# Kernel optimization log

Measured on AMD Instinct MI355X. Metric: run time of the kernel, lower is better.

Reference implementation:

```python
import jax, jax.numpy as jnp
import numpy as np

B = 2
D = 256
NH = 8
DH = D // NH
LV = 4
NP_ = 4
NL = 6
DFF = 1024
SHAPES = [(112, 112), (56, 56), (28, 28), (14, 14)]
S = sum(h * w for h, w in SHAPES)


def setup_inputs() -> dict:
    key = jax.random.key(0)
    ks = iter(jax.random.split(key, 64))
    d = {}
    for i, (h, w) in enumerate(SHAPES):
        d[f"src{i}"] = jax.random.normal(next(ks), (B, D, h, w), jnp.float32)
        d[f"pos{i}"] = jax.random.normal(next(ks), (B, D, h, w), jnp.float32)

    def W(*shape, scale=0.02):
        return jax.random.normal(next(ks), shape, jnp.float32) * scale

    d["level_embed"] = W(LV, D, scale=1.0)
    d["off_w"] = W(NL, D, NH * LV * NP_ * 2)
    d["off_b"] = W(NL, NH * LV * NP_ * 2, scale=0.5)
    d["aw_w"] = W(NL, D, NH * LV * NP_)
    d["aw_b"] = jnp.zeros((NL, NH * LV * NP_), jnp.float32)
    d["val_w"] = W(NL, D, D)
    d["val_b"] = jnp.zeros((NL, D), jnp.float32)
    d["out_w"] = W(NL, D, D)
    d["out_b"] = jnp.zeros((NL, D), jnp.float32)
    d["ln1_s"] = jnp.ones((NL, D), jnp.float32)
    d["ln1_b"] = jnp.zeros((NL, D), jnp.float32)
    d["ff1_w"] = W(NL, D, DFF)
    d["ff1_b"] = jnp.zeros((NL, DFF), jnp.float32)
    d["ff2_w"] = W(NL, DFF, D)
    d["ff2_b"] = jnp.zeros((NL, D), jnp.float32)
    d["ln2_s"] = jnp.ones((NL, D), jnp.float32)
    d["ln2_b"] = jnp.zeros((NL, D), jnp.float32)
    return d


def _ln(x, s, b):
    m = jnp.mean(x, -1, keepdims=True)
    v = jnp.mean((x - m) ** 2, -1, keepdims=True)
    return (x - m) / jnp.sqrt(v + 1e-5) * s + b


def _bilinear(v, loc, Hl, Wl):
    # v: [N, DH, Hl, Wl]; loc: [N, Q, P, 2] in [0,1] (grid_sample align_corners=False, zero padding)
    N, Dh = v.shape[0], v.shape[1]
    Q, P = loc.shape[1], loc.shape[2]
    x = loc[..., 0] * Wl - 0.5
    y = loc[..., 1] * Hl - 0.5
    x0f = jnp.floor(x)
    y0f = jnp.floor(y)
    lx = x - x0f
    ly = y - y0f
    x0 = x0f.astype(jnp.int32)
    y0 = y0f.astype(jnp.int32)
    vf = v.reshape(N, Dh, Hl * Wl)

    def g(xi, yi):
        valid = (xi >= 0) & (xi < Wl) & (yi >= 0) & (yi < Hl)
        idx = (jnp.clip(yi, 0, Hl - 1) * Wl + jnp.clip(xi, 0, Wl - 1)).reshape(N, Q * P)
        out = jnp.take_along_axis(vf, idx[:, None, :], axis=2).reshape(N, Dh, Q, P)
        return out * valid[:, None].astype(v.dtype)

    w00 = ((1 - lx) * (1 - ly))[:, None]
    w10 = (lx * (1 - ly))[:, None]
    w01 = ((1 - lx) * ly)[:, None]
    w11 = (lx * ly)[:, None]
    return g(x0, y0) * w00 + g(x0 + 1, y0) * w10 + g(x0, y0 + 1) * w01 + g(x0 + 1, y0 + 1) * w11


def _ms_deform_attn(value, loc, attn):
    # value [B,S,NH,DH], loc [B,S,NH,LV,P,2], attn [B,S,NH,LV,P]
    out = jnp.zeros((B * NH, DH, S), value.dtype)
    s0 = 0
    for l, (Hl, Wl) in enumerate(SHAPES):
        vl = value[:, s0:s0 + Hl * Wl].reshape(B, Hl, Wl, NH, DH)
        vl = vl.transpose(0, 3, 4, 1, 2).reshape(B * NH, DH, Hl, Wl)
        ll = loc[:, :, :, l].transpose(0, 2, 1, 3, 4).reshape(B * NH, S, NP_, 2)
        al = attn[:, :, :, l].transpose(0, 2, 1, 3).reshape(B * NH, S, NP_)[:, None]
        out = out + (_bilinear(vl, ll, Hl, Wl) * al).sum(-1)
        s0 += Hl * Wl
    return out.reshape(B, NH * DH, S).transpose(0, 2, 1)


def _forward(srcs, poss, level_embed, off_w, off_b, aw_w, aw_b, val_w, val_b,
             out_w, out_b, ln1_s, ln1_b, ff1_w, ff1_b, ff2_w, ff2_b, ln2_s, ln2_b):
    src = jnp.concatenate([s.reshape(B, D, -1).transpose(0, 2, 1) for s in srcs], 1)
    pos = jnp.concatenate(
        [p.reshape(B, D, -1).transpose(0, 2, 1) + level_embed[i][None, None] for i, p in enumerate(poss)], 1)
    # reference points: padding masks are all-False => valid_ratios == 1
    refs = []
    for (Hl, Wl) in SHAPES:
        gy, gx = jnp.meshgrid((jnp.arange(Hl) + 0.5) / Hl, (jnp.arange(Wl) + 0.5) / Wl, indexing="ij")
        refs.append(jnp.stack([gx.ravel(), gy.ravel()], -1))
    ref = jnp.concatenate(refs, 0)  # [S, 2]
    normalizer = jnp.array([[w, h] for (h, w) in SHAPES], jnp.float32)  # [LV, 2] = (W, H)
    x = src
    for i in range(NL):
        q = x + pos
        off = (q @ off_w[i] + off_b[i]).reshape(B, S, NH, LV, NP_, 2)
        aw = jax.nn.softmax((q @ aw_w[i] + aw_b[i]).reshape(B, S, NH, LV * NP_), -1)
        aw = aw.reshape(B, S, NH, LV, NP_)
        val = (x @ val_w[i] + val_b[i]).reshape(B, S, NH, DH)
        loc = ref[None, :, None, None, None, :] + off / normalizer[None, None, None, :, None, :]
        attn_out = _ms_deform_attn(val, loc, aw) @ out_w[i] + out_b[i]
        x = _ln(x + attn_out, ln1_s[i], ln1_b[i])
        ff = jax.nn.relu(x @ ff1_w[i] + ff1_b[i]) @ ff2_w[i] + ff2_b[i]
        x = _ln(x + ff, ln2_s[i], ln2_b[i])
    return x


def reference(src0, src1, src2, src3, pos0, pos1, pos2, pos3, level_embed,
              off_w, off_b, aw_w, aw_b, val_w, val_b, out_w, out_b,
              ln1_s, ln1_b, ff1_w, ff1_b, ff2_w, ff2_b, ln2_s, ln2_b):
    memory = _forward([src0, src1, src2, src3], [pos0, pos1, pos2, pos3], level_embed,
                      off_w, off_b, aw_w, aw_b, val_w, val_b, out_w, out_b,
                      ln1_s, ln1_b, ff1_w, ff1_b, ff2_w, ff2_b, ln2_s, ln2_b)
    spatial_shapes = jnp.array(SHAPES, jnp.int32)
    level_start_index = jnp.concatenate(
        [jnp.zeros((1,), jnp.int32), jnp.cumsum(spatial_shapes.prod(1))[:-1].astype(jnp.int32)])
    return memory, spatial_shapes, level_start_index
```

## Files before the change

### kernel.cpp

```cpp
#include <hip/hip_runtime.h>


constexpr int kB  = 2;
constexpr int kD  = 256;
constexpr int kNH = 8;
constexpr int kLV = 4;
constexpr int kNP = 4;
constexpr int kNL = 6;
constexpr int kDFF = 1024;
constexpr int kS  = 16660;
constexpr int kM  = kB * kS;
constexpr int kMp = 33408;
constexpr int kMT64 = kMp / 64;
constexpr int kMT32 = kMp / 32;

typedef short bf16x8 __attribute__((ext_vector_type(8)));
typedef float f32x4  __attribute__((ext_vector_type(4)));

__device__ __forceinline__ unsigned short f2bf(float x) {
  union { float f; unsigned int u; } v; v.f = x;
  unsigned int r = v.u + 0x7FFFu + ((v.u >> 16) & 1u);
  return (unsigned short)(r >> 16);
}
__device__ __forceinline__ float bf2f(unsigned short u) {
  union { unsigned int u; float f; } v; v.u = ((unsigned int)u) << 16;
  return v.f;
}
__device__ __forceinline__ float bflo(unsigned int u) {
  union { unsigned int u; float f; } v; v.u = u << 16;
  return v.f;
}
__device__ __forceinline__ float bfhi(unsigned int u) {
  union { unsigned int u; float f; } v; v.u = u & 0xFFFF0000u;
  return v.f;
}

#define GLOAD_LDS16(gp, lp)                                                    \
  __builtin_amdgcn_global_load_lds(                                            \
      (const __attribute__((address_space(1))) void*)(gp),                     \
      (__attribute__((address_space(3))) void*)(lp), 16, 0, 0)

__global__ __launch_bounds__(256) void build_xpos_k(
    const float* __restrict__ src, const float* __restrict__ pos,
    const float* __restrict__ lemb, float* __restrict__ xout,
    float* __restrict__ posout, unsigned short* __restrict__ xbf,
    unsigned short* __restrict__ qbf, int HW, int s0, int lvl)
{
  __shared__ float ts[32][33];
  __shared__ float tp[32][33];
  const int b  = blockIdx.z;
  const int p0 = blockIdx.x * 32, d0 = blockIdx.y * 32;
  const int tx = threadIdx.x, ty = threadIdx.y;
  for (int dd = ty; dd < 32; dd += 8) {
    int p = p0 + tx;
    if (p < HW) {
      size_t idx = ((size_t)b * kD + (d0 + dd)) * (size_t)HW + p;
      ts[dd][tx] = src[idx];
      tp[dd][tx] = pos[idx];
    }
  }
  __syncthreads();
  for (int pp = ty; pp < 32; pp += 8) {
    int p = p0 + pp, d = d0 + tx;
    if (p < HW) {
      size_t o = ((size_t)b * kS + (s0 + p)) * (size_t)kD + d;
      float x = ts[tx][pp];
      float pv = tp[tx][pp] + lemb[lvl * kD + d];
      xout[o] = x;
      posout[o] = pv;
      xbf[o] = f2bf(x);
      qbf[o] = f2bf(x + pv);
    }
  }
}

__global__ __launch_bounds__(256) void wconv_k(
    const float* __restrict__ W, unsigned short* __restrict__ Wt,
    int K, int N, int rowoff, int rowstotal)
{
  __shared__ float t[32][33];
  const int l = blockIdx.z;
  const int n0 = blockIdx.x * 32, k0 = blockIdx.y * 32;
  const int tx = threadIdx.x & 31, ty = threadIdx.x >> 5;
  const float* Wl = W + (size_t)l * K * N;
  unsigned short* Wtl = Wt + (size_t)l * rowstotal * K;
  for (int kk = ty; kk < 32; kk += 8)
    t[kk][tx] = Wl[(size_t)(k0 + kk) * N + n0 + tx];
  __syncthreads();
  for (int nn = ty; nn < 32; nn += 8)
    Wtl[(size_t)(rowoff + n0 + nn) * K + k0 + tx] = f2bf(t[tx][nn]);
}

__global__ __launch_bounds__(256) void biaspack_k(
    const float* __restrict__ ob, const float* __restrict__ ab,
    float* __restrict__ qb)
{
  int i = blockIdx.x * 256 + threadIdx.x;
  if (i >= kNL * 384) return;
  int l = i / 384, c = i - l * 384;
  qb[i] = (c < 256) ? ob[l * 256 + c] : ab[l * 128 + (c - 256)];
}

__global__ __launch_bounds__(256) void refxy_k(float* __restrict__ ref)
{
  int s = blockIdx.x * 256 + threadIdx.x;
  if (s >= kS) return;
  int ls, side;
  if (s < 12544)      { ls = s;         side = 112; }
  else if (s < 15680) { ls = s - 12544; side = 56;  }
  else if (s < 16464) { ls = s - 15680; side = 28;  }
  else                { ls = s - 16464; side = 14;  }
  const float inv = 1.0f / (float)side;
  ref[s * 2 + 0] = ((ls % side) + 0.5f) * inv;
  ref[s * 2 + 1] = ((ls / side) + 0.5f) * inv;
}

template<int RELU, int OUTBF>
__global__ __launch_bounds__(256) void hgemm64_k(
    const unsigned short* __restrict__ A, const unsigned short* __restrict__ Bt,
    const float* __restrict__ bias, void* __restrict__ Cout, int N, int K)
{
  __shared__ unsigned short As[2][64 * 32];
  __shared__ unsigned short Bs[2][128 * 32];
  const int tid = threadIdx.x;
  const int bm = blockIdx.y * 64;
  const int bn = blockIdx.x * 128;
  const int lane = tid & 63;
  const int wave = tid >> 6;
  const int wr = (wave >> 1) * 32, wc = (wave & 1) * 64;
  const int l15 = lane & 15, l4 = lane >> 4;

  f32x4 acc[2][4] = {};

  const unsigned short* A0 = A + (size_t)(bm + (tid >> 2)) * K + ((tid & 3) << 3);
  const int cb1 = 256 + tid;
  const unsigned short* B0 = Bt + (size_t)(bn + (tid >> 2)) * K + ((tid & 3) << 3);
  const unsigned short* B1 = Bt + (size_t)(bn + (cb1 >> 2)) * K + ((cb1 & 3) << 3);

#define STAGE64(buf, k0)                                                       \
  do {                                                                         \
    GLOAD_LDS16(A0 + (k0), (char*)As[buf] + tid * 16);                         \
    GLOAD_LDS16(B0 + (k0), (char*)Bs[buf] + tid * 16);                         \
    GLOAD_LDS16(B1 + (k0), (char*)Bs[buf] + cb1 * 16);                         \
  } while (0)

  STAGE64(0, 0);
  __syncthreads();
  int cur = 0;
  for (int k0 = 0; k0 < K; k0 += 32) {
    if (k0 + 32 < K) STAGE64(cur ^ 1, k0 + 32);
    bf16x8 af[2], bfr[4];
#pragma unroll
    for (int m = 0; m < 2; ++m)
      af[m] = *(const bf16x8*)&As[cur][(wr + m * 16 + l15) * 32 + l4 * 8];
#pragma unroll
    for (int n = 0; n < 4; ++n)
      bfr[n] = *(const bf16x8*)&Bs[cur][(wc + n * 16 + l15) * 32 + l4 * 8];
#pragma unroll
    for (int m = 0; m < 2; ++m)
#pragma unroll
      for (int n = 0; n < 4; ++n)
        acc[m][n] = __builtin_amdgcn_mfma_f32_16x16x32_bf16(
            af[m], bfr[n], acc[m][n], 0, 0, 0);
    __syncthreads();
    cur ^= 1;
  }
#undef STAGE64

#pragma unroll
  for (int n = 0; n < 4; ++n) {
    const int col = bn + wc + n * 16 + l15;
    const float bv = bias[col];
#pragma unroll
    for (int m = 0; m < 2; ++m) {
#pragma unroll
      for (int j = 0; j < 4; ++j) {
        const int row = bm + wr + m * 16 + l4 * 4 + j;
        float v = acc[m][n][j] + bv;
        if (RELU) v = fmaxf(v, 0.f);
        if (OUTBF)
          ((unsigned short*)Cout)[(size_t)row * N + col] = f2bf(v);
        else
          ((float*)Cout)[(size_t)row * N + col] = v;
      }
    }
  }
}

__global__ __launch_bounds__(256) void qvgemm_k(
    const unsigned short* __restrict__ Aq, const unsigned short* __restrict__ Ax,
    const unsigned short* __restrict__ Bq, const unsigned short* __restrict__ Bv,
    const float* __restrict__ biasq, const float* __restrict__ biasv,
    float* __restrict__ Cq, unsigned short* __restrict__ Cv)
{
  constexpr int K = 256;
  __shared__ unsigned short As[2][64 * 32];
  __shared__ unsigned short Bs[2][128 * 32];
  const int tid = threadIdx.x;
  const int bx = blockIdx.x;
  const bool isv = bx >= 3;
  const int bn = (isv ? bx - 3 : bx) * 128;
  const int bm = blockIdx.y * 64;
  const unsigned short* A  = isv ? Ax : Aq;
  const unsigned short* Bt = isv ? Bv : Bq;
  const float* bias = isv ? biasv : biasq;
  const int lane = tid & 63;
  const int wave = tid >> 6;
  const int wr = (wave >> 1) * 32, wc = (wave & 1) * 64;
  const int l15 = lane & 15, l4 = lane >> 4;

  f32x4 acc[2][4] = {};

  const unsigned short* A0 = A + (size_t)(bm + (tid >> 2)) * K + ((tid & 3) << 3);
  const int cb1 = 256 + tid;
  const unsigned short* B0 = Bt + (size_t)(bn + (tid >> 2)) * K + ((tid & 3) << 3);
  const unsigned short* B1 = Bt + (size_t)(bn + (cb1 >> 2)) * K + ((cb1 & 3) << 3);

#define STAGEQV(buf, k0)                                                       \
  do {                                                                         \
    GLOAD_LDS16(A0 + (k0), (char*)As[buf] + tid * 16);                         \
    GLOAD_LDS16(B0 + (k0), (char*)Bs[buf] + tid * 16);                         \
    GLOAD_LDS16(B1 + (k0), (char*)Bs[buf] + cb1 * 16);                         \
  } while (0)

  STAGEQV(0, 0);
  __syncthreads();
  int cur = 0;
#pragma unroll
  for (int k0 = 0; k0 < K; k0 += 32) {
    if (k0 + 32 < K) STAGEQV(cur ^ 1, k0 + 32);
    bf16x8 af[2], bfr[4];
#pragma unroll
    for (int m = 0; m < 2; ++m)
      af[m] = *(const bf16x8*)&As[cur][(wr + m * 16 + l15) * 32 + l4 * 8];
#pragma unroll
    for (int n = 0; n < 4; ++n)
      bfr[n] = *(const bf16x8*)&Bs[cur][(wc + n * 16 + l15) * 32 + l4 * 8];
#pragma unroll
    for (int m = 0; m < 2; ++m)
#pragma unroll
      for (int n = 0; n < 4; ++n)
        acc[m][n] = __builtin_amdgcn_mfma_f32_16x16x32_bf16(
            af[m], bfr[n], acc[m][n], 0, 0, 0);
    __syncthreads();
    cur ^= 1;
  }
#undef STAGEQV

#pragma unroll
  for (int n = 0; n < 4; ++n) {
    const int col = bn + wc + n * 16 + l15;
    const float bv = bias[col];
#pragma unroll
    for (int m = 0; m < 2; ++m) {
#pragma unroll
      for (int j = 0; j < 4; ++j) {
        const int row = bm + wr + m * 16 + l4 * 4 + j;
        float v = acc[m][n][j] + bv;
        if (isv)
          Cv[(size_t)row * 256 + col] = f2bf(v);
        else
          Cq[(size_t)row * 384 + col] = v;
      }
    }
  }
}

template<int WQ, int OUTDST>
__global__ __launch_bounds__(256) void hgemmln_k(
    const unsigned short* __restrict__ A, const unsigned short* __restrict__ Bt,
    const float* __restrict__ bias, const float* __restrict__ Rsd,
    const float* __restrict__ g, const float* __restrict__ beta,
    const float* __restrict__ posb, float* __restrict__ yout,
    unsigned short* __restrict__ xbf, unsigned short* __restrict__ qbf, int K)
{
  __shared__ unsigned short As[2][32 * 32];
  __shared__ unsigned short Bs[2][256 * 32];
  __shared__ float ssum[32][5];
  __shared__ float ssq[32][5];
  const int tid = threadIdx.x;
  const int bm = blockIdx.x * 32;
  const int lane = tid & 63;
  const int wave = tid >> 6;
  const int wc = wave * 64;
  const int l15 = lane & 15, l4 = lane >> 4;

  f32x4 acc[2][4] = {};

  const unsigned short* Aq = A + (size_t)(bm + (tid >> 2)) * K + ((tid & 3) << 3);
  const unsigned short* Bq0 = Bt + (size_t)(0 * 64 + (tid >> 2)) * K + ((tid & 3) << 3);
  const unsigned short* Bq1 = Bt + (size_t)(1 * 64 + (tid >> 2)) * K + ((tid & 3) << 3);
  const unsigned short* Bq2 = Bt + (size_t)(2 * 64 + (tid >> 2)) * K + ((tid & 3) << 3);
  const unsigned short* Bq3 = Bt + (size_t)(3 * 64 + (tid >> 2)) * K + ((tid & 3) << 3);

#define STAGE_LN(buf, k0)                                                      \
  do {                                                                         \
    if (tid < 128) GLOAD_LDS16(Aq + (k0), (char*)As[buf] + tid * 16);          \
    GLOAD_LDS16(Bq0 + (k0), (char*)Bs[buf] + (0 * 256 + tid) * 16);            \
    GLOAD_LDS16(Bq1 + (k0), (char*)Bs[buf] + (1 * 256 + tid) * 16);            \
    GLOAD_LDS16(Bq2 + (k0), (char*)Bs[buf] + (2 * 256 + tid) * 16);            \
    GLOAD_LDS16(Bq3 + (k0), (char*)Bs[buf] + (3 * 256 + tid) * 16);            \
  } while (0)

  STAGE_LN(0, 0);
  __syncthreads();
  int cur = 0;
  for (int k0 = 0; k0 < K; k0 += 32) {
    if (k0 + 32 < K) STAGE_LN(cur ^ 1, k0 + 32);
    bf16x8 af[2], bfr[4];
#pragma unroll
    for (int m = 0; m < 2; ++m)
      af[m] = *(const bf16x8*)&As[cur][(m * 16 + l15) * 32 + l4 * 8];
#pragma unroll
    for (int n = 0; n < 4; ++n)
      bfr[n] = *(const bf16x8*)&Bs[cur][(wc + n * 16 + l15) * 32 + l4 * 8];
#pragma unroll
    for (int m = 0; m < 2; ++m)
#pragma unroll
      for (int n = 0; n < 4; ++n)
        acc[m][n] = __builtin_amdgcn_mfma_f32_16x16x32_bf16(
            af[m], bfr[n], acc[m][n], 0, 0, 0);
    __syncthreads();
    cur ^= 1;
  }
#undef STAGE_LN

  float bv[4], gv[4], btv[4];
#pragma unroll
  for (int n = 0; n < 4; ++n) {
    const int col = wc + n * 16 + l15;
    bv[n] = bias[col];
    gv[n] = g[col];
    btv[n] = beta[col];
  }
#pragma unroll
  for (int m = 0; m < 2; ++m) {
#pragma unroll
    for (int j = 0; j < 4; ++j) {
      const int row = bm + m * 16 + l4 * 4 + j;
#pragma unroll
      for (int n = 0; n < 4; ++n)
        acc[m][n][j] += bv[n] + Rsd[(size_t)row * kD + wc + n * 16 + l15];
    }
  }
#pragma unroll
  for (int m = 0; m < 2; ++m) {
#pragma unroll
    for (int j = 0; j < 4; ++j) {
      float s = acc[m][0][j] + acc[m][1][j] + acc[m][2][j] + acc[m][3][j];
      float q = acc[m][0][j] * acc[m][0][j] + acc[m][1][j] * acc[m][1][j] +
                acc[m][2][j] * acc[m][2][j] + acc[m][3][j] * acc[m][3][j];
#pragma unroll
      for (int d2 = 1; d2 < 16; d2 <<= 1) {
        s += __shfl_xor(s, d2, 64);
        q += __shfl_xor(q, d2, 64);
      }
      if (l15 == 0) {
        const int r = m * 16 + l4 * 4 + j;
        ssum[r][wave] = s;
        ssq[r][wave] = q;
      }
    }
  }
  __syncthreads();
#pragma unroll
  for (int m = 0; m < 2; ++m) {
#pragma unroll
    for (int j = 0; j < 4; ++j) {
      const int r = m * 16 + l4 * 4 + j;
      const int row = bm + r;
      const float mean = (ssum[r][0] + ssum[r][1] + ssum[r][2] + ssum[r][3]) *
                         (1.0f / kD);
      const float var = (ssq[r][0] + ssq[r][1] + ssq[r][2] + ssq[r][3]) *
                        (1.0f / kD) - mean * mean;
      const float rstd = rsqrtf(var + 1e-5f);
      if (row < kM) {
#pragma unroll
        for (int n = 0; n < 4; ++n) {
          const int col = wc + n * 16 + l15;
          const float y = (acc[m][n][j] - mean) * rstd * gv[n] + btv[n];
          const size_t o = (size_t)row * kD + col;
          if (OUTDST) {
            yout[o] = y;
          } else {
            yout[o] = y;
            xbf[o] = f2bf(y);
            if (WQ) qbf[o] = f2bf(y + posb[o]);
          }
        }
      }
    }
  }
}

__global__ __launch_bounds__(256) void msdeform_k(
    const unsigned short* __restrict__ val, const float* __restrict__ qout,
    const float* __restrict__ ref, unsigned short* __restrict__ outbf)
{
  __shared__ int   sIdx[4][8][128];
  __shared__ float sW[4][8][128];
  const int bs0 = blockIdx.x * 8;
  const int tid = threadIdx.x;

#pragma unroll
  for (int it = 0; it < 4; ++it) {
    const int item = tid + it * 256;
    const int q = item >> 7;
    const int t = item & 127;
    const int bs = bs0 + q;
    const int b = bs / kS, s = bs - b * kS;
    const int l = (t & 15) >> 2;

    const float logit = qout[(size_t)bs * 384 + 256 + t];
    float mx = logit;
#pragma unroll
    for (int d2 = 1; d2 < 16; d2 <<= 1) mx = fmaxf(mx, __shfl_xor(mx, d2, 64));
    float e = __expf(logit - mx);
    float sm = e;
#pragma unroll
    for (int d2 = 1; d2 < 16; d2 <<= 1) sm += __shfl_xor(sm, d2, 64);
    const float a = e / sm;

    const float rfx = ref[s * 2 + 0];
    const float rfy = ref[s * 2 + 1];
    const int side  = 112 >> l;
    const int start = (l >= 1 ? 12544 : 0) + (l >= 2 ? 3136 : 0) + (l >= 3 ? 784 : 0);
    const float ox = qout[(size_t)bs * 384 + t * 2 + 0];
    const float oy = qout[(size_t)bs * 384 + t * 2 + 1];
    const float xx = fmaf(rfx, (float)side, ox) - 0.5f;
    const float yy = fmaf(rfy, (float)side, oy) - 0.5f;
    const float xf = floorf(xx), yf = floorf(yy);
    const float lx = xx - xf, ly = yy - yf;
    const int x0 = (int)xf, y0 = (int)yf;
    const float w00 = (1.f - lx) * (1.f - ly) * a, w10 = lx * (1.f - ly) * a;
    const float w01 = (1.f - lx) * ly * a,         w11 = lx * ly * a;
    const bool xv0 = (unsigned)x0 < (unsigned)side, xv1 = (unsigned)(x0 + 1) < (unsigned)side;
    const bool yv0 = (unsigned)y0 < (unsigned)side, yv1 = (unsigned)(y0 + 1) < (unsigned)side;
    const int cx0 = min(max(x0, 0), side - 1), cx1 = min(max(x0 + 1, 0), side - 1);
    const int cy0 = min(max(y0, 0), side - 1), cy1 = min(max(y0 + 1, 0), side - 1);
    const int rowbase = b * kS + start;
    const int t2 = (t & 15) * 8 + (t >> 4);
    sIdx[0][q][t2] = (rowbase + cy0 * side + cx0) << 9;
    sIdx[1][q][t2] = (rowbase + cy0 * side + cx1) << 9;
    sIdx[2][q][t2] = (rowbase + cy1 * side + cx0) << 9;
    sIdx[3][q][t2] = (rowbase + cy1 * side + cx1) << 9;
    sW[0][q][t2] = (xv0 && yv0) ? w00 : 0.f;
    sW[1][q][t2] = (xv1 && yv0) ? w10 : 0.f;
    sW[2][q][t2] = (xv0 && yv1) ? w01 : 0.f;
    sW[3][q][t2] = (xv1 && yv1) ? w11 : 0.f;
  }
  __syncthreads();

  const int q  = tid >> 5;
  const int h  = (tid >> 2) & 7;
  const int l4 = tid & 3;
  const char* vbase = (const char*)val + h * 64 + l4 * 16;

  float a0 = 0.f, a1 = 0.f, a2 = 0.f, a3 = 0.f;
  float a4 = 0.f, a5 = 0.f, a6 = 0.f, a7 = 0.f;
#pragma unroll
  for (int sp = 0; sp < 16; ++sp) {
    const int t2 = sp * 8 + h;
#pragma unroll
    for (int c = 0; c < 4; ++c) {
      const int off = sIdx[c][q][t2];
      const float w = sW[c][q][t2];
      const uint4 v = *(const uint4*)(vbase + off);
      a0 = fmaf(w, bflo(v.x), a0); a1 = fmaf(w, bfhi(v.x), a1);
      a2 = fmaf(w, bflo(v.y), a2); a3 = fmaf(w, bfhi(v.y), a3);
      a4 = fmaf(w, bflo(v.z), a4); a5 = fmaf(w, bfhi(v.z), a5);
      a6 = fmaf(w, bflo(v.w), a6); a7 = fmaf(w, bfhi(v.w), a7);
    }
  }
  bf16x8 o;
  o[0] = (short)f2bf(a0); o[1] = (short)f2bf(a1);
  o[2] = (short)f2bf(a2); o[3] = (short)f2bf(a3);
  o[4] = (short)f2bf(a4); o[5] = (short)f2bf(a5);
  o[6] = (short)f2bf(a6); o[7] = (short)f2bf(a7);
  *(bf16x8*)(outbf + (size_t)(bs0 + q) * 256 + h * 32 + l4 * 8) = o;
}

__global__ void tail_k(float* __restrict__ out)
{
  if (threadIdx.x == 0) {
    const size_t n = (size_t)kM * kD;
    out[n + 0] = 112.f; out[n + 1] = 112.f;
    out[n + 2] = 56.f;  out[n + 3] = 56.f;
    out[n + 4] = 28.f;  out[n + 5] = 28.f;
    out[n + 6] = 14.f;  out[n + 7] = 14.f;
    out[n + 8] = 0.f;   out[n + 9] = 12544.f;
    out[n + 10] = 15680.f; out[n + 11] = 16464.f;
  }
}

extern "C" void kernel_launch(void* const* d_in, const int* in_sizes, int n_in,
                              void* d_out, int out_size, void* d_ws, size_t ws_size,
                              hipStream_t stream)
{
  const float* src[4] = {(const float*)d_in[0], (const float*)d_in[2],
                         (const float*)d_in[4], (const float*)d_in[6]};
  const float* pos[4] = {(const float*)d_in[1], (const float*)d_in[3],
                         (const float*)d_in[5], (const float*)d_in[7]};
  const float* lemb  = (const float*)d_in[8];
  const float* off_w = (const float*)d_in[9];
  const float* off_b = (const float*)d_in[10];
  const float* aw_w  = (const float*)d_in[11];
  const float* aw_b  = (const float*)d_in[12];
  const float* val_w = (const float*)d_in[13];
  const float* val_b = (const float*)d_in[14];
  const float* out_w = (const float*)d_in[15];
  const float* out_b = (const float*)d_in[16];
  const float* ln1_s = (const float*)d_in[17];
  const float* ln1_b = (const float*)d_in[18];
  const float* ff1_w = (const float*)d_in[19];
  const float* ff1_b = (const float*)d_in[20];
  const float* ff2_w = (const float*)d_in[21];
  const float* ff2_b = (const float*)d_in[22];
  const float* ln2_s = (const float*)d_in[23];
  const float* ln2_b = (const float*)d_in[24];

  const size_t SZ = (size_t)kMp * kD;
  float* ws   = (float*)d_ws;
  float* posb = (float*)d_out;
  float* xb   = ws;
  float* R    = ws + SZ;
  float* qout = R;
  unsigned short* valbf = (unsigned short*)(R + SZ + SZ / 2);
  unsigned short* attbf = (unsigned short*)(R + 2 * SZ);
  unsigned short* ffbf  = (unsigned short*)R;
  unsigned short* qbf   = (unsigned short*)(ws + 3 * SZ);
  unsigned short* xbf   = qbf + SZ;
  unsigned short* wts   = (unsigned short*)(ws + 4 * SZ);
  unsigned short* qwT  = wts;
  unsigned short* valT = qwT + kNL * 384 * 256;
  unsigned short* outT = valT + kNL * 256 * 256;
  unsigned short* ff1T = outT + kNL * 256 * 256;
  unsigned short* ff2T = ff1T + kNL * 1024 * 256;
  float* qbias = (float*)(ff2T + kNL * 256 * 1024);
  float* reftab = qbias + kNL * 384;

  wconv_k<<<dim3(256 / 32, 256 / 32, kNL), 256, 0, stream>>>(off_w, qwT, 256, 256, 0, 384);
  wconv_k<<<dim3(128 / 32, 256 / 32, kNL), 256, 0, stream>>>(aw_w,  qwT, 256, 128, 256, 384);
  wconv_k<<<dim3(256 / 32, 256 / 32, kNL), 256, 0, stream>>>(val_w, valT, 256, 256, 0, 256);
  wconv_k<<<dim3(256 / 32, 256 / 32, kNL), 256, 0, stream>>>(out_w, outT, 256, 256, 0, 256);
  wconv_k<<<dim3(1024 / 32, 256 / 32, kNL), 256, 0, stream>>>(ff1_w, ff1T, 256, 1024, 0, 1024);
  wconv_k<<<dim3(256 / 32, 1024 / 32, kNL), 256, 0, stream>>>(ff2_w, ff2T, 1024, 256, 0, 256);
  biaspack_k<<<(kNL * 384 + 255) / 256, 256, 0, stream>>>(off_b, aw_b, qbias);
  refxy_k<<<(kS + 255) / 256, 256, 0, stream>>>(reftab);

  const int sides[4]  = {112, 56, 28, 14};
  const int starts[4] = {0, 12544, 15680, 16464};
  for (int l = 0; l < 4; ++l) {
    int HW = sides[l] * sides[l];
    dim3 g((HW + 31) / 32, kD / 32, kB);
    build_xpos_k<<<g, dim3(32, 8), 0, stream>>>(src[l], pos[l], lemb, xb, posb,
                                                xbf, qbf, HW, starts[l], l);
  }

  const dim3 blk(256);
  for (int i = 0; i < kNL; ++i) {
    qvgemm_k<<<dim3(5, kMT64), blk, 0, stream>>>(
        qbf, xbf, qwT + (size_t)i * 384 * 256, valT + (size_t)i * 256 * 256,
        qbias + i * 384, val_b + i * 256, qout, valbf);
    msdeform_k<<<kM / 8, blk, 0, stream>>>(valbf, qout, reftab, attbf);
    hgemmln_k<0, 0><<<kMT32, blk, 0, stream>>>(
        attbf, outT + (size_t)i * 256 * 256, out_b + i * 256, xb,
        ln1_s + i * kD, ln1_b + i * kD, nullptr, xb, xbf, nullptr, 256);
    hgemm64_k<1, 1><<<dim3(8, kMT64), blk, 0, stream>>>(
        xbf, ff1T + (size_t)i * 1024 * 256, ff1_b + i * 1024, ffbf, 1024, 256);
    if (i < kNL - 1) {
      hgemmln_k<1, 0><<<kMT32, blk, 0, stream>>>(
          ffbf, ff2T + (size_t)i * 256 * 1024, ff2_b + i * 256, xb,
          ln2_s + i * kD, ln2_b + i * kD, posb, xb, xbf, qbf, 1024);
    } else {
      hgemmln_k<0, 1><<<kMT32, blk, 0, stream>>>(
          ffbf, ff2T + (size_t)i * 256 * 1024, ff2_b + i * 256, xb,
          ln2_s + i * kD, ln2_b + i * kD, nullptr, (float*)d_out, nullptr,
          nullptr, 1024);
    }
  }

  tail_k<<<1, 64, 0, stream>>>((float*)d_out);
}
```

Before: 1.443 ms.

## Deepen GEMM prefetch to two stages with explicit vmcnt waits and raw barriers

The three bf16 MFMA GEMM kernels now prefetch two K-tiles ahead instead of one. Each iteration waits on a partial vmcnt count rather than doing a full __syncthreads drain, so one global-to-LDS load stays in flight while the current tile is computed. The loads for tile k+2 are issued right after the compute barrier. This relies on hand-counted vmcnt values, which must match the number of outstanding global_load_lds ops per wave (3, or 4/5 in the LN kernel). A wrong count or a compiler-inserted load would corrupt the data or cause a race.

```diff
diff --git a/kernel.cpp b/kernel.cpp
--- a/kernel.cpp
+++ b/kernel.cpp
@@ -40,6 +40,8 @@
       (const __attribute__((address_space(1))) void*)(gp),                     \
       (__attribute__((address_space(3))) void*)(lp), 16, 0, 0)
 
+#define SBARRIER() asm volatile("s_barrier" ::: "memory")
+
 __global__ __launch_bounds__(256) void build_xpos_k(
     const float* __restrict__ src, const float* __restrict__ pos,
     const float* __restrict__ lemb, float* __restrict__ xout,
@@ -144,11 +146,15 @@
     GLOAD_LDS16(B1 + (k0), (char*)Bs[buf] + cb1 * 16);                         \
   } while (0)
 
+  const int nt = K >> 5;
   STAGE64(0, 0);
-  __syncthreads();
-  int cur = 0;
-  for (int k0 = 0; k0 < K; k0 += 32) {
-    if (k0 + 32 < K) STAGE64(cur ^ 1, k0 + 32);
+  STAGE64(1, 32);
+  for (int k = 0; k < nt; ++k) {
+    if (k + 1 < nt) asm volatile("s_waitcnt vmcnt(3)" ::: "memory");
+    else            asm volatile("s_waitcnt vmcnt(0)" ::: "memory");
+    SBARRIER();
+    __builtin_amdgcn_sched_barrier(0);
+    const int cur = k & 1;
     bf16x8 af[2], bfr[4];
 #pragma unroll
     for (int m = 0; m < 2; ++m)
@@ -162,8 +168,8 @@
       for (int n = 0; n < 4; ++n)
         acc[m][n] = __builtin_amdgcn_mfma_f32_16x16x32_bf16(
             af[m], bfr[n], acc[m][n], 0, 0, 0);
-    __syncthreads();
-    cur ^= 1;
+    SBARRIER();
+    if (k + 2 < nt) STAGE64(cur, (k + 2) * 32);
   }
 #undef STAGE64
 
@@ -223,12 +229,15 @@
     GLOAD_LDS16(B1 + (k0), (char*)Bs[buf] + cb1 * 16);                         \
   } while (0)
 
+  const int nt = K >> 5;
   STAGEQV(0, 0);
-  __syncthreads();
-  int cur = 0;
-#pragma unroll
-  for (int k0 = 0; k0 < K; k0 += 32) {
-    if (k0 + 32 < K) STAGEQV(cur ^ 1, k0 + 32);
+  STAGEQV(1, 32);
+  for (int k = 0; k < nt; ++k) {
+    if (k + 1 < nt) asm volatile("s_waitcnt vmcnt(3)" ::: "memory");
+    else            asm volatile("s_waitcnt vmcnt(0)" ::: "memory");
+    SBARRIER();
+    __builtin_amdgcn_sched_barrier(0);
+    const int cur = k & 1;
     bf16x8 af[2], bfr[4];
 #pragma unroll
     for (int m = 0; m < 2; ++m)
@@ -242,8 +251,8 @@
       for (int n = 0; n < 4; ++n)
         acc[m][n] = __builtin_amdgcn_mfma_f32_16x16x32_bf16(
             af[m], bfr[n], acc[m][n], 0, 0, 0);
-    __syncthreads();
-    cur ^= 1;
+    SBARRIER();
+    if (k + 2 < nt) STAGEQV(cur, (k + 2) * 32);
   }
 #undef STAGEQV
 
@@ -302,11 +311,19 @@
     GLOAD_LDS16(Bq3 + (k0), (char*)Bs[buf] + (3 * 256 + tid) * 16);            \
   } while (0)
 
+  const int nt = K >> 5;
   STAGE_LN(0, 0);
-  __syncthreads();
-  int cur = 0;
-  for (int k0 = 0; k0 < K; k0 += 32) {
-    if (k0 + 32 < K) STAGE_LN(cur ^ 1, k0 + 32);
+  STAGE_LN(1, 32);
+  for (int k = 0; k < nt; ++k) {
+    if (k + 1 < nt) {
+      if (wave < 2) asm volatile("s_waitcnt vmcnt(5)" ::: "memory");
+      else          asm volatile("s_waitcnt vmcnt(4)" ::: "memory");
+    } else {
+      asm volatile("s_waitcnt vmcnt(0)" ::: "memory");
+    }
+    SBARRIER();
+    __builtin_amdgcn_sched_barrier(0);
+    const int cur = k & 1;
     bf16x8 af[2], bfr[4];
 #pragma unroll
     for (int m = 0; m < 2; ++m)
@@ -320,8 +337,8 @@
       for (int n = 0; n < 4; ++n)
         acc[m][n] = __builtin_amdgcn_mfma_f32_16x16x32_bf16(
             af[m], bfr[n], acc[m][n], 0, 0, 0);
-    __syncthreads();
-    cur ^= 1;
+    SBARRIER();
+    if (k + 2 < nt) STAGE_LN(cur, (k + 2) * 32);
   }
 #undef STAGE_LN
 
```

Result: no change. 1.425 ms (-1.2%).
